# Kernel optimization log

Measured on AMD Instinct MI355X. Metric: run time of the kernel, lower is better.

## Reference

```python
import jax, jax.numpy as jnp
import numpy as np

N_FEATURES = 1_000_000
N_FIELDS = 50
EMB_DIM = 64
ATT_DIM = EMB_DIM // 2
BATCH = 2048


def setup_inputs() -> dict:
    key = jax.random.key(0)
    ks = jax.random.split(key, 7)
    features = jax.random.randint(ks[0], (BATCH, N_FIELDS), 0, N_FEATURES)
    emb_table = jax.random.normal(ks[1], (N_FEATURES, EMB_DIM), dtype=jnp.float32) * 0.01
    coeff_table = jax.random.normal(ks[2], (N_FEATURES, 1), dtype=jnp.float32) * 0.01
    bias = jnp.zeros((1,), dtype=jnp.float32)
    # kaiming normal for relu: std = sqrt(2/fan_in)
    att_w = jax.random.normal(ks[3], (ATT_DIM, EMB_DIM), dtype=jnp.float32) * np.sqrt(2.0 / EMB_DIM)
    att_b = jnp.zeros((ATT_DIM,), dtype=jnp.float32)
    p = jax.random.normal(ks[4], (ATT_DIM, 1), dtype=jnp.float32)
    w = jnp.ones((EMB_DIM, 1), dtype=jnp.float32)
    return {"features": features, "emb_table": emb_table, "coeff_table": coeff_table,
            "bias": bias, "att_w": att_w, "att_b": att_b, "p": p, "w": w}


def reference(features, emb_table, coeff_table, bias, att_w, att_b, p, w):
    # Dropout layers in eval mode (identity).
    emb = emb_table[features]            # [B, F, D]
    coeff = coeff_table[features]        # [B, F, 1]
    iu, ju = jnp.triu_indices(N_FIELDS, k=1)
    # pairwise hadamard products in row-major (i,j) order matching the loop
    interactions = emb[:, iu, :] * emb[:, ju, :]   # [B, P, D], P = F*(F-1)/2
    # attention MLP: relu(x @ att_w^T + att_b) @ p -> scores over interactions
    hidden = jax.nn.relu(jnp.einsum('bpd,ad->bpa', interactions, att_w) + att_b)
    scores = jnp.einsum('bpa,ao->bpo', hidden, p)  # [B, P, 1]
    att = jax.nn.softmax(scores, axis=1)           # softmax over interaction dim
    pooled = jnp.sum(interactions * att, axis=1)   # [B, D]
    interaction_part = (pooled @ w).reshape(-1)    # [B]
    linear_part = jnp.sum(coeff, axis=1).reshape(-1)
    return interaction_part + linear_part + bias
```

## Files before the change

kernel.cpp:

```cpp
#include <hip/hip_runtime.h>
#include <hip/hip_fp16.h>
#include <math.h>

#define NFIELDS 50
#define EMBD 64
#define ATTD 32
#define NPAIRS 1225
#define NPAD 1248
#define NTILES 39
#define NTHREADS 256
#define NWAVES 4
#define MAXT 10
#define NFPAD 51

typedef _Float16 f16x8 __attribute__((ext_vector_type(8)));
typedef _Float16 f16x2 __attribute__((ext_vector_type(2)));
typedef float f32x16 __attribute__((ext_vector_type(16)));

union F16x8U { f16x8 v; f16x2 h2[4]; unsigned int u[4]; uint4 q; };
union U32F { unsigned int u; f16x2 h; };

__device__ __forceinline__ float dot2acc(f16x2 a, f16x2 b, float c) {
#if __has_builtin(__builtin_amdgcn_fdot2)
    return __builtin_amdgcn_fdot2(a, b, c, false);
#else
    return c + (float)a[0] * (float)b[0] + (float)a[1] * (float)b[1];
#endif
}

__launch_bounds__(NTHREADS, 3)
__global__ void afm_kernel(const int* __restrict__ features,
                           const float* __restrict__ emb_table,
                           const float* __restrict__ coeff_table,
                           const float* __restrict__ bias,
                           const float* __restrict__ att_w,
                           const float* __restrict__ att_b,
                           const float* __restrict__ pvec,
                           const float* __restrict__ wvec,
                           float* __restrict__ out)
{
    __shared__ __align__(16) unsigned short emb3[8][NFPAD][8];
    __shared__ unsigned short pair_s[NPAD];
    __shared__ int   feat_s[NFIELDS];
    __shared__ float coeff_s[NFIELDS];
    __shared__ float red_max[NWAVES], red_sum[NWAVES], red_sumt[NWAVES];

    const int b    = blockIdx.x;
    const int tid  = threadIdx.x;
    const int lane = tid & 63;
    const int wid  = tid >> 6;
    const int col  = lane & 31;
    const int h    = lane >> 5;
    const int h4   = h * 4;

    if (tid < NFIELDS) {
        int f = features[b * NFIELDS + tid];
        feat_s[tid] = f;
        coeff_s[tid] = coeff_table[f];
    }
    if (tid >= 64 && tid < 64 + NFIELDS - 1) {
        int i = tid - 64;
        int off = i * NFIELDS - (i * (i + 1)) / 2;
        int cnt = NFIELDS - 1 - i;
        for (int k = 0; k < cnt; ++k)
            pair_s[off + k] = (unsigned short)((i << 8) | (i + 1 + k));
    }
    if (tid == 113) {
        for (int q = NPAIRS; q < NPAD; ++q) pair_s[q] = (unsigned short)1;
    }

    f16x8 afragW[4];
    f16x2 w2[16];
    #pragma unroll
    for (int c = 0; c < 4; ++c) {
        const int d0 = c * 16 + h * 8;
        const float4 wa0 = *reinterpret_cast<const float4*>(&att_w[col * EMBD + d0]);
        const float4 wa1 = *reinterpret_cast<const float4*>(&att_w[col * EMBD + d0 + 4]);
        F16x8U bf;
        bf.v[0] = (_Float16)wa0.x; bf.v[1] = (_Float16)wa0.y;
        bf.v[2] = (_Float16)wa0.z; bf.v[3] = (_Float16)wa0.w;
        bf.v[4] = (_Float16)wa1.x; bf.v[5] = (_Float16)wa1.y;
        bf.v[6] = (_Float16)wa1.z; bf.v[7] = (_Float16)wa1.w;
        afragW[c] = bf.v;
        const float4 wv0 = *reinterpret_cast<const float4*>(&wvec[d0]);
        const float4 wv1 = *reinterpret_cast<const float4*>(&wvec[d0 + 4]);
        f16x2 t0; t0[0] = (_Float16)wv0.x; t0[1] = (_Float16)wv0.y; w2[c * 4 + 0] = t0;
        f16x2 t1; t1[0] = (_Float16)wv0.z; t1[1] = (_Float16)wv0.w; w2[c * 4 + 1] = t1;
        f16x2 t2; t2[0] = (_Float16)wv1.x; t2[1] = (_Float16)wv1.y; w2[c * 4 + 2] = t2;
        f16x2 t3; t3[0] = (_Float16)wv1.z; t3[1] = (_Float16)wv1.w; w2[c * 4 + 3] = t3;
    }
    float attb_r[16], p_r[16];
    #pragma unroll
    for (int reg = 0; reg < 16; ++reg) {
        const int r = (reg & 3) + 8 * (reg >> 2) + 4 * h;
        attb_r[reg] = att_b[r];
        p_r[reg]    = pvec[r];
    }
    __syncthreads();

    for (int idx = tid; idx < NFIELDS * 16; idx += NTHREADS) {
        const int f  = idx >> 4;
        const int d0 = (idx & 15) * 4;
        const float4 v = *reinterpret_cast<const float4*>(
            &emb_table[(size_t)feat_s[f] * EMBD + d0]);
        const int c  = d0 >> 4;
        const int hh = (d0 >> 3) & 1;
        const int e0 = d0 & 7;
        U32F t0, t1;
        t0.h[0] = (_Float16)v.x; t0.h[1] = (_Float16)v.y;
        t1.h[0] = (_Float16)v.z; t1.h[1] = (_Float16)v.w;
        uint2 pk; pk.x = t0.u; pk.y = t1.u;
        *reinterpret_cast<uint2*>(&emb3[hh * 4 + c][f][e0]) = pk;
    }
    __syncthreads();

    float scv[MAXT], tv[MAXT];
    #pragma unroll
    for (int k = 0; k < MAXT; ++k) { scv[k] = -INFINITY; tv[k] = 0.f; }

    #pragma unroll
    for (int tt = 0; tt < MAXT; ++tt) {
        const int tile = wid + tt * NWAVES;
        if (tile < NTILES) {
            const int pidx = tile * 32 + col;
            const unsigned int ij = pair_s[pidx];
            const int fi = ij >> 8;
            const int fj = ij & 255;

            f32x16 acc;
            #pragma unroll
            for (int k = 0; k < 16; ++k) acc[k] = 0.f;

            float t_half = 0.f;
            #pragma unroll
            for (int c = 0; c < 4; ++c) {
                F16x8U ai, aj;
                ai.q = *reinterpret_cast<const uint4*>(&emb3[h4 + c][fi][0]);
                aj.q = *reinterpret_cast<const uint4*>(&emb3[h4 + c][fj][0]);
                const f16x2 x0 = ai.h2[0] * aj.h2[0];
                const f16x2 x1 = ai.h2[1] * aj.h2[1];
                const f16x2 x2 = ai.h2[2] * aj.h2[2];
                const f16x2 x3 = ai.h2[3] * aj.h2[3];
                t_half = dot2acc(x0, w2[c * 4 + 0], t_half);
                t_half = dot2acc(x1, w2[c * 4 + 1], t_half);
                t_half = dot2acc(x2, w2[c * 4 + 2], t_half);
                t_half = dot2acc(x3, w2[c * 4 + 3], t_half);
                F16x8U bf;
                bf.h2[0] = x0; bf.h2[1] = x1; bf.h2[2] = x2; bf.h2[3] = x3;
                acc = __builtin_amdgcn_mfma_f32_32x32x16_f16(afragW[c], bf.v, acc, 0, 0, 0);
            }

            float sp = 0.f;
            #pragma unroll
            for (int reg = 0; reg < 16; ++reg)
                sp = fmaf(fmaxf(acc[reg] + attb_r[reg], 0.f), p_r[reg], sp);
            const float sc = sp + __shfl_xor(sp, 32, 64);
            const float tf = t_half + __shfl_xor(t_half, 32, 64);
            if (h == 0 && pidx < NPAIRS) { scv[tt] = sc; tv[tt] = tf; }
        }
    }

    float lmax = -INFINITY;
    #pragma unroll
    for (int k = 0; k < MAXT; ++k) lmax = fmaxf(lmax, scv[k]);
    #pragma unroll
    for (int m = 1; m < 64; m <<= 1) lmax = fmaxf(lmax, __shfl_xor(lmax, m, 64));
    if (lane == 0) red_max[wid] = lmax;
    __syncthreads();
    const float gmax = fmaxf(fmaxf(red_max[0], red_max[1]),
                             fmaxf(red_max[2], red_max[3]));

    float lsum = 0.f, lsumt = 0.f;
    #pragma unroll
    for (int k = 0; k < MAXT; ++k) {
        float e = __expf(scv[k] - gmax);
        lsum  += e;
        lsumt += e * tv[k];
    }
    #pragma unroll
    for (int m = 1; m < 64; m <<= 1) {
        lsum  += __shfl_xor(lsum, m, 64);
        lsumt += __shfl_xor(lsumt, m, 64);
    }
    if (lane == 0) { red_sum[wid] = lsum; red_sumt[wid] = lsumt; }
    __syncthreads();

    if (tid == 0) {
        float S  = red_sum[0] + red_sum[1] + red_sum[2] + red_sum[3];
        float ST = red_sumt[0] + red_sumt[1] + red_sumt[2] + red_sumt[3];
        float csum = 0.f;
        for (int i = 0; i < NFIELDS; ++i) csum += coeff_s[i];
        out[b] = ST / S + csum + bias[0];
    }
}

extern "C" void kernel_launch(void* const* d_in, const int* in_sizes, int n_in,
                              void* d_out, int out_size, void* d_ws, size_t ws_size,
                              hipStream_t stream) {
    const int*   features    = (const int*)d_in[0];
    const float* emb_table   = (const float*)d_in[1];
    const float* coeff_table = (const float*)d_in[2];
    const float* bias        = (const float*)d_in[3];
    const float* att_w       = (const float*)d_in[4];
    const float* att_b       = (const float*)d_in[5];
    const float* pvec        = (const float*)d_in[6];
    const float* wvec        = (const float*)d_in[7];
    float* out = (float*)d_out;

    const int batch = in_sizes[0] / NFIELDS;
    afm_kernel<<<batch, NTHREADS, 0, stream>>>(
        features, emb_table, coeff_table, bias, att_w, att_b, pvec, wvec, out);
}
```

Before: 36.28 us.

## Use online softmax, parallel pair-index build, and higher occupancy target

Replaces the per-thread score/value arrays and two-pass max/sum softmax with an online running max/sum merged across lanes and waves, which drops one barrier and the MAXT-sized register arrays. Pads the tile count to 40 so the loop needs no bounds branch, and folds att_b into the MFMA accumulator initialisation. The pair table is now filled by all threads using a closed-form sqrt inversion instead of a few serial loops. The coeff sum and bias are reduced with a wave shuffle, and launch bounds rise to 4 blocks per CU. The cost is extra exp calls per tile and during the merges, plus possible float error in the sqrt-based index math.

Measured after the change: 35.94 us. Within noise of the previous version (-1.0%).

```diff
diff --git a/kernel.cpp b/kernel.cpp
--- a/kernel.cpp
+++ b/kernel.cpp
@@ -4,13 +4,13 @@
 
 #define NFIELDS 50
 #define EMBD 64
-#define ATTD 32
 #define NPAIRS 1225
-#define NPAD 1248
-#define NTILES 39
+#define NTILEPAD 40
+#define NPAD (NTILEPAD * 32)
 #define NTHREADS 256
 #define NWAVES 4
-#define MAXT 10
+#define NITER (NTILEPAD / NWAVES)
+#define QPT (NPAD / NTHREADS)
 #define NFPAD 51
 
 typedef _Float16 f16x8 __attribute__((ext_vector_type(8)));
@@ -28,7 +28,9 @@
 #endif
 }
 
-__launch_bounds__(NTHREADS, 3)
+#define MNEG (-1e30f)
+
+__launch_bounds__(NTHREADS, 4)
 __global__ void afm_kernel(const int* __restrict__ features,
                            const float* __restrict__ emb_table,
                            const float* __restrict__ coeff_table,
@@ -42,8 +44,8 @@
     __shared__ __align__(16) unsigned short emb3[8][NFPAD][8];
     __shared__ unsigned short pair_s[NPAD];
     __shared__ int   feat_s[NFIELDS];
-    __shared__ float coeff_s[NFIELDS];
-    __shared__ float red_max[NWAVES], red_sum[NWAVES], red_sumt[NWAVES];
+    __shared__ float red_m[NWAVES], red_s[NWAVES], red_st[NWAVES];
+    __shared__ float red_csum;
 
     const int b    = blockIdx.x;
     const int tid  = threadIdx.x;
@@ -53,20 +55,32 @@
     const int h    = lane >> 5;
     const int h4   = h * 4;
 
+    int myfeat = 0;
     if (tid < NFIELDS) {
-        int f = features[b * NFIELDS + tid];
-        feat_s[tid] = f;
-        coeff_s[tid] = coeff_table[f];
-    }
-    if (tid >= 64 && tid < 64 + NFIELDS - 1) {
-        int i = tid - 64;
-        int off = i * NFIELDS - (i * (i + 1)) / 2;
-        int cnt = NFIELDS - 1 - i;
-        for (int k = 0; k < cnt; ++k)
-            pair_s[off + k] = (unsigned short)((i << 8) | (i + 1 + k));
-    }
-    if (tid == 113) {
-        for (int q = NPAIRS; q < NPAD; ++q) pair_s[q] = (unsigned short)1;
+        myfeat = features[b * NFIELDS + tid];
+        feat_s[tid] = myfeat;
+    }
+
+    #pragma unroll
+    for (int k = 0; k < QPT; ++k) {
+        const int q = tid * QPT + k;
+        int i = 0, j = 1;
+        if (q < NPAIRS) {
+            const float s = sqrtf((float)(9801 - 8 * q));
+            i = (int)((99.0f - s) * 0.5f);
+            const int off = i * NFIELDS - ((i * (i + 1)) >> 1);
+            j = i + 1 + (q - off);
+        }
+        pair_s[q] = (unsigned short)((i << 8) | j);
+    }
+
+    if (wid == 0) {
+        float cacc = 0.f;
+        if (tid < NFIELDS)       cacc = coeff_table[myfeat];
+        else if (tid == NFIELDS) cacc = bias[0];
+        #pragma unroll
+        for (int m = 1; m < 64; m <<= 1) cacc += __shfl_xor(cacc, m, 64);
+        if (tid == 0) red_csum = cacc;
     }
 
     f16x8 afragW[4];
@@ -114,83 +128,83 @@
     }
     __syncthreads();
 
-    float scv[MAXT], tv[MAXT];
-    #pragma unroll
-    for (int k = 0; k < MAXT; ++k) { scv[k] = -INFINITY; tv[k] = 0.f; }
-
-    #pragma unroll
-    for (int tt = 0; tt < MAXT; ++tt) {
+    float m_run = MNEG, s_run = 0.f, st_run = 0.f;
+
+    #pragma unroll 2
+    for (int tt = 0; tt < NITER; ++tt) {
         const int tile = wid + tt * NWAVES;
-        if (tile < NTILES) {
-            const int pidx = tile * 32 + col;
-            const unsigned int ij = pair_s[pidx];
-            const int fi = ij >> 8;
-            const int fj = ij & 255;
-
-            f32x16 acc;
-            #pragma unroll
-            for (int k = 0; k < 16; ++k) acc[k] = 0.f;
-
-            float t_half = 0.f;
-            #pragma unroll
-            for (int c = 0; c < 4; ++c) {
-                F16x8U ai, aj;
-                ai.q = *reinterpret_cast<const uint4*>(&emb3[h4 + c][fi][0]);
-                aj.q = *reinterpret_cast<const uint4*>(&emb3[h4 + c][fj][0]);
-                const f16x2 x0 = ai.h2[0] * aj.h2[0];
-                const f16x2 x1 = ai.h2[1] * aj.h2[1];
-                const f16x2 x2 = ai.h2[2] * aj.h2[2];
-                const f16x2 x3 = ai.h2[3] * aj.h2[3];
-                t_half = dot2acc(x0, w2[c * 4 + 0], t_half);
-                t_half = dot2acc(x1, w2[c * 4 + 1], t_half);
-                t_half = dot2acc(x2, w2[c * 4 + 2], t_half);
-                t_half = dot2acc(x3, w2[c * 4 + 3], t_half);
-                F16x8U bf;
-                bf.h2[0] = x0; bf.h2[1] = x1; bf.h2[2] = x2; bf.h2[3] = x3;
-                acc = __builtin_amdgcn_mfma_f32_32x32x16_f16(afragW[c], bf.v, acc, 0, 0, 0);
-            }
-
-            float sp = 0.f;
-            #pragma unroll
-            for (int reg = 0; reg < 16; ++reg)
-                sp = fmaf(fmaxf(acc[reg] + attb_r[reg], 0.f), p_r[reg], sp);
-            const float sc = sp + __shfl_xor(sp, 32, 64);
-            const float tf = t_half + __shfl_xor(t_half, 32, 64);
-            if (h == 0 && pidx < NPAIRS) { scv[tt] = sc; tv[tt] = tf; }
+        const int pidx = tile * 32 + col;
+        const unsigned int ij = pair_s[pidx];
+        const int fi = ij >> 8;
+        const int fj = ij & 255;
+
+        f32x16 acc;
+        #pragma unroll
+        for (int reg = 0; reg < 16; ++reg) acc[reg] = attb_r[reg];
+
+        float t_half = 0.f;
+        #pragma unroll
+        for (int c = 0; c < 4; ++c) {
+            F16x8U ai, aj;
+            ai.q = *reinterpret_cast<const uint4*>(&emb3[h4 + c][fi][0]);
+            aj.q = *reinterpret_cast<const uint4*>(&emb3[h4 + c][fj][0]);
+            const f16x2 x0 = ai.h2[0] * aj.h2[0];
+            const f16x2 x1 = ai.h2[1] * aj.h2[1];
+            const f16x2 x2 = ai.h2[2] * aj.h2[2];
+            const f16x2 x3 = ai.h2[3] * aj.h2[3];
+            t_half = dot2acc(x0, w2[c * 4 + 0], t_half);
+            t_half = dot2acc(x1, w2[c * 4 + 1], t_half);
+            t_half = dot2acc(x2, w2[c * 4 + 2], t_half);
+            t_half = dot2acc(x3, w2[c * 4 + 3], t_half);
+            F16x8U bf;
+            bf.h2[0] = x0; bf.h2[1] = x1; bf.h2[2] = x2; bf.h2[3] = x3;
+            acc = __builtin_amdgcn_mfma_f32_32x32x16_f16(afragW[c], bf.v, acc, 0, 0, 0);
         }
-    }
-
-    float lmax = -INFINITY;
-    #pragma unroll
-    for (int k = 0; k < MAXT; ++k) lmax = fmaxf(lmax, scv[k]);
-    #pragma unroll
-    for (int m = 1; m < 64; m <<= 1) lmax = fmaxf(lmax, __shfl_xor(lmax, m, 64));
-    if (lane == 0) red_max[wid] = lmax;
+
+        float sp = 0.f;
+        #pragma unroll
+        for (int reg = 0; reg < 16; ++reg)
+            sp = fmaf(fmaxf(acc[reg], 0.f), p_r[reg], sp);
+        const float sc = sp + __shfl_xor(sp, 32, 64);
+        const float tf = t_half + __shfl_xor(t_half, 32, 64);
+
+        const bool valid = (pidx < NPAIRS);
+        const float scm = valid ? sc : MNEG;
+        const float mn  = fmaxf(m_run, scm);
+        const float scale = __expf(m_run - mn);
+        const float e     = valid ? __expf(sc - mn) : 0.f;
+        s_run  = s_run  * scale + e;
+        st_run = st_run * scale + e * tf;
+        m_run  = mn;
+    }
+
+    #pragma unroll
+    for (int m = 1; m < 64; m <<= 1) {
+        const float m2  = __shfl_xor(m_run, m, 64);
+        const float s2  = __shfl_xor(s_run, m, 64);
+        const float st2 = __shfl_xor(st_run, m, 64);
+        const float mn  = fmaxf(m_run, m2);
+        const float ea  = __expf(m_run - mn);
+        const float eb  = __expf(m2 - mn);
+        s_run  = s_run * ea + s2 * eb;
+        st_run = st_run * ea + st2 * eb;
+        m_run  = mn;
+    }
+    if (lane == 0) { red_m[wid] = m_run; red_s[wid] = s_run; red_st[wid] = st_run; }
     __syncthreads();
-    const float gmax = fmaxf(fmaxf(red_max[0], red_max[1]),
-                             fmaxf(red_max[2], red_max[3]));
-
-    float lsum = 0.f, lsumt = 0.f;
-    #pragma unroll
-    for (int k = 0; k < MAXT; ++k) {
-        float e = __expf(scv[k] - gmax);
-        lsum  += e;
-        lsumt += e * tv[k];
-    }
-    #pragma unroll
-    for (int m = 1; m < 64; m <<= 1) {
-        lsum  += __shfl_xor(lsum, m, 64);
-        lsumt += __shfl_xor(lsumt, m, 64);
-    }
-    if (lane == 0) { red_sum[wid] = lsum; red_sumt[wid] = lsumt; }
-    __syncthreads();
 
     if (tid == 0) {
-        float S  = red_sum[0] + red_sum[1] + red_sum[2] + red_sum[3];
-        float ST = red_sumt[0] + red_sumt[1] + red_sumt[2] + red_sumt[3];
-        float csum = 0.f;
-        for (int i = 0; i < NFIELDS; ++i) csum += coeff_s[i];
-        out[b] = ST / S + csum + bias[0];
+        float M = red_m[0], S = red_s[0], ST = red_st[0];
+        #pragma unroll
+        for (int wq = 1; wq < NWAVES; ++wq) {
+            const float mn = fmaxf(M, red_m[wq]);
+            const float ea = __expf(M - mn);
+            const float eb = __expf(red_m[wq] - mn);
+            S  = S * ea + red_s[wq] * eb;
+            ST = ST * ea + red_st[wq] * eb;
+            M  = mn;
+        }
+        out[b] = ST / S + red_csum;
     }
 }
 
```
